# Kernel optimization log

Hardware: AMD Instinct MI355X
Metric: run time of the kernel (lower is better)

## Reference

```python
import jax, jax.numpy as jnp
import numpy as np

B, S, D, H, DH = 2, 1024, 1024, 16, 64
SCALE = 1.0 / np.sqrt(DH)


def setup_inputs() -> dict:
    key = jax.random.key(0)
    ks = jax.random.split(key, 9)
    return {
        "x": jax.random.normal(ks[0], (B, S, D), jnp.float32),
        "qkv_w": jax.random.normal(ks[1], (3 * H * DH, D), jnp.float32) * 0.02,
        "out_w": jax.random.normal(ks[2], (D, H * DH), jnp.float32) * 0.02,
        "bias_p": jax.random.uniform(ks[3], (H, 1, 1), jnp.float32) * 2.0,
        "bias_a": jax.random.uniform(ks[4], (H, 1, 1), jnp.float32),
        "mlp_w1": jax.random.normal(ks[5], (H, 2 * H), jnp.float32) * 0.1,
        "mlp_b1": jnp.zeros((H,), jnp.float32),
        "mlp_w2": jax.random.normal(ks[6], (H, H), jnp.float32) * 0.1,
        "mlp_b2": jnp.zeros((H,), jnp.float32),
    }


def reference(x, qkv_w, out_w, bias_p, bias_a, mlp_w1, mlp_b1, mlp_w2, mlp_b2):
    # qkv projection: torch Linear => x @ W.T
    qkv = (x @ qkv_w.T).reshape(B, S, 3, H, DH)
    q = qkv[:, :, 0].transpose(0, 2, 1, 3)  # [B,H,S,DH]
    k = qkv[:, :, 1].transpose(0, 2, 1, 3)
    v = qkv[:, :, 2].transpose(0, 2, 1, 3)

    scores = jnp.einsum('bhqd,bhkd->bhqk', q, k) * SCALE  # [B,H,S,S]

    # Kerple additive bias: -p * log1p(a * |i-j|), per head
    p = jnp.clip(bias_p, 0.01)
    a = jnp.clip(bias_a, 0.01)
    pos = jnp.arange(S, dtype=jnp.float32)
    dist = jnp.abs(pos[None, :] - pos[:, None])  # [S,S]
    kb = -p * jnp.log1p(a * dist)  # [H,S,S]

    # DAPE refinement MLP over per-(i,j) head features
    z = jnp.concatenate(
        [scores, jnp.broadcast_to(kb[None], (B, H, S, S))], axis=1
    ).transpose(0, 2, 3, 1)  # [B,S,S,2H]
    hdn = jax.nn.gelu(z @ mlp_w1.T + mlp_b1, approximate=False)  # [B,S,S,H]
    refine = (hdn @ mlp_w2.T + mlp_b2).transpose(0, 3, 1, 2)  # [B,H,S,S]

    scores = scores + kb[None] + refine
    attn = jax.nn.softmax(scores, axis=-1)  # dropout is identity in eval

    out = jnp.einsum('bhqk,bhkd->bhqd', attn, v)  # [B,H,S,DH]
    out = out.transpose(0, 2, 1, 3).reshape(B, S, H * DH)
    return out @ out_w.T
```

## Files before the change

### kernel.cpp

```cpp
#include <hip/hip_runtime.h>
#include <math.h>

#define Bsz 2
#define Ssz 1024
#define Dsz 1024
#define Hn 16
#define DHsz 64
#define QKV3 3072
#define SCALE 0.125f

typedef __bf16 bf16;
typedef bf16 bf16x8 __attribute__((ext_vector_type(8)));
typedef bf16 bf16x4 __attribute__((ext_vector_type(4)));
typedef float f32x4 __attribute__((ext_vector_type(4)));

#define MFMA(a, b, c) __builtin_amdgcn_mfma_f32_16x16x32_bf16(a, b, c, 0, 0, 0)
#define LDT 72

__global__ void cast_hi(const float* __restrict__ src, bf16* __restrict__ hi, int n) {
  int idx = (blockIdx.x * 256 + threadIdx.x) * 4;
  if (idx >= n) return;
  float4 v = *(const float4*)(src + idx);
  bf16x4 hv = {(bf16)v.x, (bf16)v.y, (bf16)v.z, (bf16)v.w};
  *(bf16x4*)(hi + idx) = hv;
}

__global__ void kb_table(const float* __restrict__ bias_p, const float* __restrict__ bias_a,
                         float* __restrict__ kbtt) {
  int idx = blockIdx.x * 256 + threadIdx.x;
  int d = idx >> 4, h = idx & 15;
  float p = fmaxf(bias_p[h], 0.01f), a = fmaxf(bias_a[h], 0.01f);
  kbtt[idx] = -p * log1pf(a * (float)d);
}

__global__ void tk_table(const float* __restrict__ kbtt, const float* __restrict__ w1,
                         const float* __restrict__ b1, float2* __restrict__ tk) {
  int idx = blockIdx.x * 256 + threadIdx.x;
  int o = idx >> 4, n = idx & 15;
  int d = o - 1024; if (d < 0) d = -d; if (d > 1023) d = 1023;
  float t1 = b1[n];
#pragma unroll
  for (int h = 0; h < 16; ++h) t1 += w1[n * 32 + 16 + h] * kbtt[d * 16 + h];
  tk[idx] = make_float2(t1, kbtt[d * 16 + n]);
}

__global__ void wfrag(const float* __restrict__ w1, const float* __restrict__ w2,
                      bf16* __restrict__ wf) {
  int lane = threadIdx.x;
  int l15 = lane & 15, q8 = (lane >> 4) << 3;
  bf16x8 w1d, w2a;
#pragma unroll
  for (int e = 0; e < 8; ++e) {
    int k = q8 + e;
    if (k < 16) {
      w1d[e] = (bf16)w1[l15 * 32 + k];
    } else {
      float w = w1[l15 * 32 + k - 16];
      w1d[e] = (bf16)(w - (float)(bf16)w);
    }
    w2a[e] = (bf16)w2[l15 * 16 + (k & 15)];
  }
  *(bf16x8*)(wf + lane * 8) = w1d;
  *(bf16x8*)(wf + 512 + lane * 8) = w2a;
}

__global__ __launch_bounds__(256, 3) void k1_qkv(const bf16* __restrict__ A,
                                                 const bf16* __restrict__ B,
                                                 bf16* __restrict__ C) {
  __shared__ __align__(16) bf16 sA[128 * LDT];
  __shared__ __align__(16) bf16 sB[96 * LDT];
  const int tid = threadIdx.x;
  const int lane = tid & 63, wv = tid >> 6;
  const int wr = wv >> 1, wc = wv & 1;
  const int l15 = lane & 15, q8 = (lane >> 4) << 3, q4 = (lane >> 4) << 2;
  const int m0 = blockIdx.y * 128, n0 = blockIdx.x * 96;
  const int r0 = tid >> 3, c8 = (tid & 7) << 3;

  f32x4 acc[4][3];
#pragma unroll
  for (int t = 0; t < 4; ++t)
#pragma unroll
    for (int u = 0; u < 3; ++u)
#pragma unroll
      for (int r = 0; r < 4; ++r) acc[t][u][r] = 0.f;

  bf16x8 rA[4], rB[3];
#define K1_LOAD(kt)                                                         \
  {                                                                         \
    _Pragma("unroll") for (int c = 0; c < 4; ++c)                           \
      rA[c] = *(const bf16x8*)(A + (size_t)(m0 + c * 32 + r0) * Dsz + (kt) + c8);  \
    _Pragma("unroll") for (int c = 0; c < 3; ++c)                           \
      rB[c] = *(const bf16x8*)(B + (size_t)(n0 + c * 32 + r0) * Dsz + (kt) + c8);  \
  }

  K1_LOAD(0)
  for (int kt = 0; kt < Dsz; kt += 64) {
    __syncthreads();
#pragma unroll
    for (int c = 0; c < 4; ++c) *(bf16x8*)&sA[(c * 32 + r0) * LDT + c8] = rA[c];
#pragma unroll
    for (int c = 0; c < 3; ++c) *(bf16x8*)&sB[(c * 32 + r0) * LDT + c8] = rB[c];
    __syncthreads();
    if (kt + 64 < Dsz) K1_LOAD(kt + 64)
#pragma unroll
    for (int ks = 0; ks < 64; ks += 32) {
      bf16x8 fa[4], fb[3];
#pragma unroll
      for (int t = 0; t < 4; ++t)
        fa[t] = *(const bf16x8*)&sA[(wr * 64 + t * 16 + l15) * LDT + ks + q8];
#pragma unroll
      for (int u = 0; u < 3; ++u)
        fb[u] = *(const bf16x8*)&sB[(wc * 48 + u * 16 + l15) * LDT + ks + q8];
#pragma unroll
      for (int t = 0; t < 4; ++t)
#pragma unroll
        for (int u = 0; u < 3; ++u) acc[t][u] = MFMA(fa[t], fb[u], acc[t][u]);
    }
  }
#pragma unroll
  for (int t = 0; t < 4; ++t)
#pragma unroll
    for (int u = 0; u < 3; ++u) {
      int col = n0 + wc * 48 + u * 16 + l15;
#pragma unroll
      for (int r = 0; r < 4; ++r) {
        int row = m0 + wr * 64 + t * 16 + q4 + r;
        C[(size_t)row * QKV3 + col] = (bf16)acc[t][u][r];
      }
    }
#undef K1_LOAD
}

__global__ void pack_vt(const bf16* __restrict__ qkv, bf16* __restrict__ vt) {
  __shared__ __align__(16) bf16 T[64 * LDT];
  const int tid = threadIdx.x;
  const int bh = blockIdx.y, b = bh >> 4, h = bh & 15;
  const int j0 = blockIdx.x * 64;
#pragma unroll
  for (int c = 0; c < 2; ++c) {
    int lin = c * 256 + tid;
    int jr = lin >> 3, d8 = (lin & 7) << 3;
    bf16x8 v = *(const bf16x8*)(qkv + (size_t)(b * Ssz + j0 + jr) * QKV3 + 2048 + h * DHsz + d8);
#pragma unroll
    for (int e = 0; e < 8; ++e) T[(d8 + e) * LDT + jr] = v[e];
  }
  __syncthreads();
#pragma unroll
  for (int c = 0; c < 2; ++c) {
    int lin = c * 256 + tid;
    int d = lin >> 3, j8 = (lin & 7) << 3;
    bf16x8 o = *(const bf16x8*)&T[d * LDT + j8];
    *(bf16x8*)(vt + ((size_t)(b * Hn + h) * DHsz + d) * Ssz + j0 + j8) = o;
  }
}

__global__ __launch_bounds__(256, 3) void k2_qk(const bf16* __restrict__ qkv,
                                                bf16* __restrict__ scores) {
  __shared__ __align__(16) bf16 sA[128 * LDT], sB[128 * LDT];
  const int tid = threadIdx.x;
  const int lane = tid & 63, wv = tid >> 6;
  const int wr = wv >> 1, wc = wv & 1;
  const int l15 = lane & 15, q8 = (lane >> 4) << 3, q4 = (lane >> 4) << 2;
  const int z = blockIdx.z, b = z >> 4, h = z & 15;
  const int i0 = blockIdx.y * 128, j0 = blockIdx.x * 128;
  const bf16* Ab = qkv + (size_t)b * Ssz * QKV3 + h * DHsz;
  const bf16* Bb = Ab + Ssz;
  const int r0 = tid >> 3, c8 = (tid & 7) << 3;
#pragma unroll
  for (int c = 0; c < 4; ++c) {
    int row = c * 32 + r0;
    *(bf16x8*)&sA[row * LDT + c8] = *(const bf16x8*)(Ab + (size_t)(i0 + row) * QKV3 + c8);
    *(bf16x8*)&sB[row * LDT + c8] = *(const bf16x8*)(Bb + (size_t)(j0 + row) * QKV3 + c8);
  }
  __syncthreads();
  f32x4 acc[4][4];
#pragma unroll
  for (int t = 0; t < 4; ++t)
#pragma unroll
    for (int u = 0; u < 4; ++u)
#pragma unroll
      for (int r = 0; r < 4; ++r) acc[t][u][r] = 0.f;
#pragma unroll
  for (int ks = 0; ks < 64; ks += 32) {
    bf16x8 fa[4], fb[4];
#pragma unroll
    for (int t = 0; t < 4; ++t) fa[t] = *(const bf16x8*)&sA[(wr * 64 + t * 16 + l15) * LDT + ks + q8];
#pragma unroll
    for (int u = 0; u < 4; ++u) fb[u] = *(const bf16x8*)&sB[(wc * 64 + u * 16 + l15) * LDT + ks + q8];
#pragma unroll
    for (int t = 0; t < 4; ++t)
#pragma unroll
      for (int u = 0; u < 4; ++u) acc[t][u] = MFMA(fa[t], fb[u], acc[t][u]);
  }
  bf16* dstp = scores + ((size_t)(b * Hn + h) << 20);
#pragma unroll
  for (int t = 0; t < 4; ++t)
#pragma unroll
    for (int u = 0; u < 4; ++u) {
      int col = j0 + wc * 64 + u * 16 + l15;
#pragma unroll
      for (int r = 0; r < 4; ++r) {
        int row = i0 + wr * 64 + t * 16 + q4 + r;
        dstp[((size_t)row << 10) + col] = (bf16)(acc[t][u][r] * SCALE);
      }
    }
}

__device__ __forceinline__ float gelu_fast(float x) {
  float z = fabsf(x) * 0.70710678118654752f;
  float t = __builtin_amdgcn_rcpf(fmaf(0.3275911f, z, 1.0f));
  float poly = t * fmaf(t, fmaf(t, fmaf(t, fmaf(t, 1.061405429f, -1.453152027f),
                                        1.421413741f), -0.284496736f), 0.254829592f);
  float erfa = 1.0f - poly * __expf(-z * z);
  float erfs = copysignf(erfa, x);
  return 0.5f * x * (1.0f + erfs);
}

#define SHS 264
#define LGS 264

__global__ __launch_bounds__(256, 5) void dape_softmax(bf16* scores,
                                                       const float2* __restrict__ tk,
                                                       const bf16* __restrict__ wf,
                                                       const float* __restrict__ b2,
                                                       float* __restrict__ sums) {
  const int c = blockIdx.x;
  const int i = blockIdx.y;
  const int b = blockIdx.z;
  const int tid = threadIdx.x;
  const int lane = tid & 63, wv = tid >> 6;
  const int l15 = lane & 15, q = lane >> 4;
  const int q8 = q << 3, q4 = q << 2;

  __shared__ bf16 sH[Hn][SHS];
  __shared__ float lgt[Hn][LGS];
  __shared__ __align__(16) bf16 hdnS[4][16][40];

  const bf16x8 w1d = *(const bf16x8*)(wf + lane * 8);
  const bf16x8 w2a = *(const bf16x8*)(wf + 512 + lane * 8);
  const float bias2 = b2[l15];

  if (lane < 32) {
    int row = lane >> 1, col = 16 + (lane & 1) * 8;
    *(bf16x8*)&hdnS[wv][row][col] = (bf16x8){};
  }

  const int jw = wv * 64;
  const bf16* srow = scores + ((size_t)(b * Hn) << 20) + ((size_t)i << 10) + c * 256;
#pragma unroll
  for (int t = 0; t < 2; ++t) {
    int h = t * 8 + (lane >> 3);
    int col = jw + (lane & 7) * 8;
    *(bf16x8*)&sH[h][col] = *(const bf16x8*)(srow + ((size_t)h << 20) + col);
  }

  const float2* tkp = tk + ((size_t)(c * 256 + jw + q4 - i + 1024) << 4) + l15;

  for (int jt = 0; jt < 4; ++jt) {
    const int j0c = jw + jt * 16;
    bf16x8 a1;
#pragma unroll
    for (int e = 0; e < 8; ++e) a1[e] = sH[(q8 + e) & 15][j0c + l15];
    float2 tkv[4];
#pragma unroll
    for (int r = 0; r < 4; ++r) tkv[r] = tkp[r * 16];
    f32x4 c1 = {tkv[0].x, tkv[1].x, tkv[2].x, tkv[3].x};
    c1 = MFMA(a1, w1d, c1);
#pragma unroll
    for (int r = 0; r < 4; ++r) hdnS[wv][q4 + r][l15] = (bf16)gelu_fast(c1[r]);
    bf16x8 a2 = *(const bf16x8*)&hdnS[wv][l15][q8];
    f32x4 c2 = {bias2, bias2, bias2, bias2};
    c2 = MFMA(a2, w2a, c2);
    bf16x4 sc4 = *(const bf16x4*)&sH[l15][j0c + q4];
    f32x4 lg;
#pragma unroll
    for (int r = 0; r < 4; ++r) lg[r] = (float)sc4[r] + tkv[r].y + c2[r];
    *(f32x4*)&lgt[l15][j0c + q4] = lg;
    tkp += 256;
  }
  __syncthreads();

#pragma unroll
  for (int hh = 0; hh < 4; ++hh) {
    const int h = wv * 4 + hh;
    f32x4 v0 = *(const f32x4*)&lgt[h][lane * 4];
    float s = 0.f;
#pragma unroll
    for (int e = 0; e < 4; ++e) { v0[e] = __expf(v0[e]); s += v0[e]; }
#pragma unroll
    for (int off = 32; off > 0; off >>= 1) s += __shfl_xor(s, off, 64);
    bf16* dst = scores + ((size_t)(b * Hn + h) << 20) + ((size_t)i << 10) + c * 256;
    bf16x4 p0 = {(bf16)v0[0], (bf16)v0[1], (bf16)v0[2], (bf16)v0[3]};
    *(bf16x4*)(dst + lane * 4) = p0;
    if (lane == 0) sums[((((b << 10) + i) << 4) + h) * 4 + c] = s;
  }
}

__global__ __launch_bounds__(256, 4) void k4_av(const bf16* __restrict__ attn,
                                                const bf16* __restrict__ vt,
                                                const float* __restrict__ sums,
                                                bf16* __restrict__ aout) {
  __shared__ __align__(16) bf16 sA[64 * LDT], sB[64 * LDT];
  const int tid = threadIdx.x;
  const int lane = tid & 63, wv = tid >> 6;
  const int wr = wv >> 1, wc = wv & 1;
  const int l15 = lane & 15, q8 = (lane >> 4) << 3, q4 = (lane >> 4) << 2;
  const int i0 = blockIdx.x * 64, h = blockIdx.y, b = blockIdx.z;
  const bf16* Ab = attn + ((size_t)(b * Hn + h) << 20) + ((size_t)i0 << 10);
  const bf16* Bb = vt + (size_t)(b * Hn + h) * DHsz * Ssz;
  const int r0 = tid >> 3, c8 = (tid & 7) << 3;
  f32x4 acc[2][2];
#pragma unroll
  for (int t = 0; t < 2; ++t)
#pragma unroll
    for (int u = 0; u < 2; ++u)
#pragma unroll
      for (int r = 0; r < 4; ++r) acc[t][u][r] = 0.f;
  bf16x8 rA[2], rB[2];
#define K4_LOAD(kt)                                               \
  {                                                               \
    _Pragma("unroll") for (int c = 0; c < 2; ++c) {               \
      int row = c * 32 + r0;                                      \
      rA[c] = *(const bf16x8*)(Ab + ((size_t)row << 10) + (kt) + c8); \
      rB[c] = *(const bf16x8*)(Bb + ((size_t)row << 10) + (kt) + c8); \
    }                                                             \
  }
  K4_LOAD(0)
  for (int kt = 0; kt < Ssz; kt += 64) {
    __syncthreads();
#pragma unroll
    for (int c = 0; c < 2; ++c) {
      int row = c * 32 + r0;
      *(bf16x8*)&sA[row * LDT + c8] = rA[c];
      *(bf16x8*)&sB[row * LDT + c8] = rB[c];
    }
    __syncthreads();
    if (kt + 64 < Ssz) K4_LOAD(kt + 64)
#pragma unroll
    for (int ks = 0; ks < 64; ks += 32) {
      bf16x8 fa[2], fb[2];
#pragma unroll
      for (int t = 0; t < 2; ++t) fa[t] = *(const bf16x8*)&sA[(wr * 32 + t * 16 + l15) * LDT + ks + q8];
#pragma unroll
      for (int u = 0; u < 2; ++u) fb[u] = *(const bf16x8*)&sB[(wc * 32 + u * 16 + l15) * LDT + ks + q8];
#pragma unroll
      for (int t = 0; t < 2; ++t)
#pragma unroll
        for (int u = 0; u < 2; ++u) acc[t][u] = MFMA(fa[t], fb[u], acc[t][u]);
    }
  }
#pragma unroll
  for (int t = 0; t < 2; ++t)
#pragma unroll
    for (int r = 0; r < 4; ++r) {
      int row = i0 + wr * 32 + t * 16 + q4 + r;
      f32x4 sv = *(const f32x4*)&sums[((((b << 10) + row) << 4) + h) * 4];
      float inv = 1.f / (sv[0] + sv[1] + sv[2] + sv[3]);
#pragma unroll
      for (int u = 0; u < 2; ++u) {
        int d = wc * 32 + u * 16 + l15;
        aout[(size_t)(b * Ssz + row) * Dsz + h * DHsz + d] = (bf16)(acc[t][u][r] * inv);
      }
    }
#undef K4_LOAD
}

__global__ __launch_bounds__(256, 4) void k5_out(const bf16* __restrict__ A,
                                                 const bf16* __restrict__ B,
                                                 float* __restrict__ C) {
  __shared__ __align__(16) bf16 sA[64 * LDT], sB[64 * LDT];
  const int tid = threadIdx.x;
  const int lane = tid & 63, wv = tid >> 6;
  const int wr = wv >> 1, wc = wv & 1;
  const int l15 = lane & 15, q8 = (lane >> 4) << 3, q4 = (lane >> 4) << 2;
  const int m0 = blockIdx.y * 64, n0 = blockIdx.x * 64;
  const int r0 = tid >> 3, c8 = (tid & 7) << 3;
  f32x4 acc[2][2];
#pragma unroll
  for (int t = 0; t < 2; ++t)
#pragma unroll
    for (int u = 0; u < 2; ++u)
#pragma unroll
      for (int r = 0; r < 4; ++r) acc[t][u][r] = 0.f;
  bf16x8 rA[2], rB[2];
#define K5_LOAD(kt)                                                       \
  {                                                                       \
    _Pragma("unroll") for (int c = 0; c < 2; ++c) {                       \
      int row = c * 32 + r0;                                              \
      rA[c] = *(const bf16x8*)(A + (size_t)(m0 + row) * Dsz + (kt) + c8);   \
      rB[c] = *(const bf16x8*)(B + (size_t)(n0 + row) * Dsz + (kt) + c8);   \
    }                                                                     \
  }
  K5_LOAD(0)
  for (int kt = 0; kt < Dsz; kt += 64) {
    __syncthreads();
#pragma unroll
    for (int c = 0; c < 2; ++c) {
      int row = c * 32 + r0;
      *(bf16x8*)&sA[row * LDT + c8] = rA[c];
      *(bf16x8*)&sB[row * LDT + c8] = rB[c];
    }
    __syncthreads();
    if (kt + 64 < Dsz) K5_LOAD(kt + 64)
#pragma unroll
    for (int ks = 0; ks < 64; ks += 32) {
      bf16x8 fa[2], fb[2];
#pragma unroll
      for (int t = 0; t < 2; ++t) fa[t] = *(const bf16x8*)&sA[(wr * 32 + t * 16 + l15) * LDT + ks + q8];
#pragma unroll
      for (int u = 0; u < 2; ++u) fb[u] = *(const bf16x8*)&sB[(wc * 32 + u * 16 + l15) * LDT + ks + q8];
#pragma unroll
      for (int t = 0; t < 2; ++t)
#pragma unroll
        for (int u = 0; u < 2; ++u) acc[t][u] = MFMA(fa[t], fb[u], acc[t][u]);
    }
  }
#pragma unroll
  for (int t = 0; t < 2; ++t)
#pragma unroll
    for (int u = 0; u < 2; ++u) {
      int col = n0 + wc * 32 + u * 16 + l15;
#pragma unroll
      for (int r = 0; r < 4; ++r) {
        int row = m0 + wr * 32 + t * 16 + q4 + r;
        C[(size_t)row * Dsz + col] = acc[t][u][r];
      }
    }
#undef K5_LOAD
}

extern "C" void kernel_launch(void* const* d_in, const int* in_sizes, int n_in,
                              void* d_out, int out_size, void* d_ws, size_t ws_size,
                              hipStream_t stream) {
  const float* x      = (const float*)d_in[0];
  const float* qkv_w  = (const float*)d_in[1];
  const float* out_w  = (const float*)d_in[2];
  const float* bias_p = (const float*)d_in[3];
  const float* bias_a = (const float*)d_in[4];
  const float* w1     = (const float*)d_in[5];
  const float* b1     = (const float*)d_in[6];
  const float* w2     = (const float*)d_in[7];
  const float* b2     = (const float*)d_in[8];
  float* out = (float*)d_out;

  char* ws = (char*)d_ws;
  const size_t MB = 1ull << 20;
  bf16* ow_h   = (bf16*)(ws + 0 * MB);
  bf16* qkv_bf = (bf16*)(ws + 2 * MB);
  bf16* v_t    = (bf16*)(ws + 14 * MB);
  bf16* aout   = (bf16*)(ws + 18 * MB);
  float* kbtt  = (float*)(ws + 22 * MB);
  float* sums  = (float*)(ws + 22 * MB + 65536);
  bf16* wf     = (bf16*)(ws + 22 * MB + 589824);
  float2* tk   = (float2*)(ws + 22 * MB + 655360);
  bf16* x_h    = (bf16*)(ws + 23 * MB);
  bf16* w_h    = (bf16*)(ws + 27 * MB);
  bf16* sc_bf  = (bf16*)(ws + 23 * MB);

  cast_hi<<<2048, 256, 0, stream>>>(x, x_h, Bsz * Ssz * Dsz);
  cast_hi<<<3072, 256, 0, stream>>>(qkv_w, w_h, QKV3 * Dsz);
  cast_hi<<<1024, 256, 0, stream>>>(out_w, ow_h, Dsz * Dsz);
  kb_table<<<64, 256, 0, stream>>>(bias_p, bias_a, kbtt);
  tk_table<<<128, 256, 0, stream>>>(kbtt, w1, b1, tk);
  wfrag<<<1, 64, 0, stream>>>(w1, w2, wf);

  k1_qkv<<<dim3(QKV3 / 96, (Bsz * Ssz) / 128), 256, 0, stream>>>(x_h, w_h, qkv_bf);
  pack_vt<<<dim3(Ssz / 64, Bsz * Hn), 256, 0, stream>>>(qkv_bf, v_t);

  k2_qk<<<dim3(Ssz / 128, Ssz / 128, Bsz * Hn), 256, 0, stream>>>(qkv_bf, sc_bf);
  dape_softmax<<<dim3(4, Ssz, Bsz), 256, 0, stream>>>(sc_bf, tk, wf, b2, sums);
  k4_av<<<dim3(Ssz / 64, Hn, Bsz), 256, 0, stream>>>(sc_bf, v_t, sums, aout);

  k5_out<<<dim3(Dsz / 64, (Bsz * Ssz) / 64), 256, 0, stream>>>(aout, ow_h, out);
}
```

Measured before the change: 202.9 us.

## Merge setup kernels and load GEMM fragments directly from global memory

Combines the three cast kernels into one launch and folds the kerple table, the tk table and the weight-fragment prep into a single kernel, which cuts six setup launches to two. The QK, AV and output-projection GEMMs now load MFMA fragments straight from global memory into registers and drop the LDS staging and __syncthreads. AV and the output projection double-buffer the next K tile in registers. This removes LDS traffic and barriers but gives up the coalesced cooperative loads, so global access patterns get more scattered and register pressure rises.

```diff
diff --git a/kernel.cpp b/kernel.cpp
--- a/kernel.cpp
+++ b/kernel.cpp
@@ -17,51 +17,60 @@
 #define MFMA(a, b, c) __builtin_amdgcn_mfma_f32_16x16x32_bf16(a, b, c, 0, 0, 0)
 #define LDT 72
 
-__global__ void cast_hi(const float* __restrict__ src, bf16* __restrict__ hi, int n) {
-  int idx = (blockIdx.x * 256 + threadIdx.x) * 4;
-  if (idx >= n) return;
+__global__ void cast3(const float* __restrict__ x, const float* __restrict__ qw,
+                      const float* __restrict__ ow, bf16* __restrict__ xh,
+                      bf16* __restrict__ wh, bf16* __restrict__ owh) {
+  int bid = blockIdx.x;
+  const float* src;
+  bf16* dst;
+  int base;
+  if (bid < 2048) { src = x;  dst = xh;  base = bid * 1024; }
+  else if (bid < 5120) { src = qw; dst = wh;  base = (bid - 2048) * 1024; }
+  else { src = ow; dst = owh; base = (bid - 5120) * 1024; }
+  int idx = base + threadIdx.x * 4;
   float4 v = *(const float4*)(src + idx);
   bf16x4 hv = {(bf16)v.x, (bf16)v.y, (bf16)v.z, (bf16)v.w};
-  *(bf16x4*)(hi + idx) = hv;
-}
-
-__global__ void kb_table(const float* __restrict__ bias_p, const float* __restrict__ bias_a,
-                         float* __restrict__ kbtt) {
-  int idx = blockIdx.x * 256 + threadIdx.x;
-  int d = idx >> 4, h = idx & 15;
-  float p = fmaxf(bias_p[h], 0.01f), a = fmaxf(bias_a[h], 0.01f);
-  kbtt[idx] = -p * log1pf(a * (float)d);
-}
-
-__global__ void tk_table(const float* __restrict__ kbtt, const float* __restrict__ w1,
-                         const float* __restrict__ b1, float2* __restrict__ tk) {
+  *(bf16x4*)(dst + idx) = hv;
+}
+
+__global__ void tkw(const float* __restrict__ bias_p, const float* __restrict__ bias_a,
+                    const float* __restrict__ w1, const float* __restrict__ b1,
+                    const float* __restrict__ w2, float2* __restrict__ tk,
+                    bf16* __restrict__ wf) {
+  if (blockIdx.x == 128) {
+    int lane = threadIdx.x;
+    if (lane < 64) {
+      int l15 = lane & 15, q8 = (lane >> 4) << 3;
+      bf16x8 w1d, w2a;
+#pragma unroll
+      for (int e = 0; e < 8; ++e) {
+        int k = q8 + e;
+        if (k < 16) {
+          w1d[e] = (bf16)w1[l15 * 32 + k];
+        } else {
+          float w = w1[l15 * 32 + k - 16];
+          w1d[e] = (bf16)(w - (float)(bf16)w);
+        }
+        w2a[e] = (bf16)w2[l15 * 16 + (k & 15)];
+      }
+      *(bf16x8*)(wf + lane * 8) = w1d;
+      *(bf16x8*)(wf + 512 + lane * 8) = w2a;
+    }
+    return;
+  }
   int idx = blockIdx.x * 256 + threadIdx.x;
   int o = idx >> 4, n = idx & 15;
   int d = o - 1024; if (d < 0) d = -d; if (d > 1023) d = 1023;
-  float t1 = b1[n];
-#pragma unroll
-  for (int h = 0; h < 16; ++h) t1 += w1[n * 32 + 16 + h] * kbtt[d * 16 + h];
-  tk[idx] = make_float2(t1, kbtt[d * 16 + n]);
-}
-
-__global__ void wfrag(const float* __restrict__ w1, const float* __restrict__ w2,
-                      bf16* __restrict__ wf) {
-  int lane = threadIdx.x;
-  int l15 = lane & 15, q8 = (lane >> 4) << 3;
-  bf16x8 w1d, w2a;
-#pragma unroll
-  for (int e = 0; e < 8; ++e) {
-    int k = q8 + e;
-    if (k < 16) {
-      w1d[e] = (bf16)w1[l15 * 32 + k];
-    } else {
-      float w = w1[l15 * 32 + k - 16];
-      w1d[e] = (bf16)(w - (float)(bf16)w);
-    }
-    w2a[e] = (bf16)w2[l15 * 16 + (k & 15)];
-  }
-  *(bf16x8*)(wf + lane * 8) = w1d;
-  *(bf16x8*)(wf + 512 + lane * 8) = w2a;
+  float dd = (float)d;
+  float t1 = b1[n], kbn = 0.f;
+#pragma unroll
+  for (int h = 0; h < 16; ++h) {
+    float p = fmaxf(bias_p[h], 0.01f), a = fmaxf(bias_a[h], 0.01f);
+    float kb = -p * log1pf(a * dd);
+    t1 += w1[n * 32 + 16 + h] * kb;
+    if (h == n) kbn = kb;
+  }
+  tk[idx] = make_float2(t1, kbn);
 }
 
 __global__ __launch_bounds__(256, 3) void k1_qkv(const bf16* __restrict__ A,
@@ -156,23 +165,23 @@
 
 __global__ __launch_bounds__(256, 3) void k2_qk(const bf16* __restrict__ qkv,
                                                 bf16* __restrict__ scores) {
-  __shared__ __align__(16) bf16 sA[128 * LDT], sB[128 * LDT];
   const int tid = threadIdx.x;
   const int lane = tid & 63, wv = tid >> 6;
   const int wr = wv >> 1, wc = wv & 1;
   const int l15 = lane & 15, q8 = (lane >> 4) << 3, q4 = (lane >> 4) << 2;
   const int z = blockIdx.z, b = z >> 4, h = z & 15;
   const int i0 = blockIdx.y * 128, j0 = blockIdx.x * 128;
-  const bf16* Ab = qkv + (size_t)b * Ssz * QKV3 + h * DHsz;
-  const bf16* Bb = Ab + Ssz;
-  const int r0 = tid >> 3, c8 = (tid & 7) << 3;
-#pragma unroll
-  for (int c = 0; c < 4; ++c) {
-    int row = c * 32 + r0;
-    *(bf16x8*)&sA[row * LDT + c8] = *(const bf16x8*)(Ab + (size_t)(i0 + row) * QKV3 + c8);
-    *(bf16x8*)&sB[row * LDT + c8] = *(const bf16x8*)(Bb + (size_t)(j0 + row) * QKV3 + c8);
-  }
-  __syncthreads();
+  const bf16* Ab = qkv + (size_t)(b * Ssz + i0 + wr * 64 + l15) * QKV3 + h * DHsz + q8;
+  const bf16* Bb = qkv + (size_t)(b * Ssz + j0 + wc * 64 + l15) * QKV3 + Ssz + h * DHsz + q8;
+
+  bf16x8 fa[2][4], fb[2][4];
+#pragma unroll
+  for (int s = 0; s < 2; ++s)
+#pragma unroll
+    for (int t = 0; t < 4; ++t) {
+      fa[s][t] = *(const bf16x8*)(Ab + (size_t)(t * 16) * QKV3 + s * 32);
+      fb[s][t] = *(const bf16x8*)(Bb + (size_t)(t * 16) * QKV3 + s * 32);
+    }
   f32x4 acc[4][4];
 #pragma unroll
   for (int t = 0; t < 4; ++t)
@@ -181,17 +190,12 @@
 #pragma unroll
       for (int r = 0; r < 4; ++r) acc[t][u][r] = 0.f;
 #pragma unroll
-  for (int ks = 0; ks < 64; ks += 32) {
-    bf16x8 fa[4], fb[4];
-#pragma unroll
-    for (int t = 0; t < 4; ++t) fa[t] = *(const bf16x8*)&sA[(wr * 64 + t * 16 + l15) * LDT + ks + q8];
-#pragma unroll
-    for (int u = 0; u < 4; ++u) fb[u] = *(const bf16x8*)&sB[(wc * 64 + u * 16 + l15) * LDT + ks + q8];
+  for (int s = 0; s < 2; ++s)
 #pragma unroll
     for (int t = 0; t < 4; ++t)
 #pragma unroll
-      for (int u = 0; u < 4; ++u) acc[t][u] = MFMA(fa[t], fb[u], acc[t][u]);
-  }
+      for (int u = 0; u < 4; ++u) acc[t][u] = MFMA(fa[s][t], fb[s][u], acc[t][u]);
+
   bf16* dstp = scores + ((size_t)(b * Hn + h) << 20);
 #pragma unroll
   for (int t = 0; t < 4; ++t)
@@ -300,15 +304,16 @@
                                                 const bf16* __restrict__ vt,
                                                 const float* __restrict__ sums,
                                                 bf16* __restrict__ aout) {
-  __shared__ __align__(16) bf16 sA[64 * LDT], sB[64 * LDT];
   const int tid = threadIdx.x;
   const int lane = tid & 63, wv = tid >> 6;
   const int wr = wv >> 1, wc = wv & 1;
   const int l15 = lane & 15, q8 = (lane >> 4) << 3, q4 = (lane >> 4) << 2;
   const int i0 = blockIdx.x * 64, h = blockIdx.y, b = blockIdx.z;
-  const bf16* Ab = attn + ((size_t)(b * Hn + h) << 20) + ((size_t)i0 << 10);
-  const bf16* Bb = vt + (size_t)(b * Hn + h) * DHsz * Ssz;
-  const int r0 = tid >> 3, c8 = (tid & 7) << 3;
+  const bf16* a0p = attn + ((size_t)(b * Hn + h) << 20) + ((size_t)(i0 + wr * 32 + l15) << 10) + q8;
+  const bf16* a1p = a0p + (16 << 10);
+  const bf16* b0p = vt + (size_t)(b * Hn + h) * DHsz * Ssz + ((size_t)(wc * 32 + l15) << 10) + q8;
+  const bf16* b1p = b0p + (16 << 10);
+
   f32x4 acc[2][2];
 #pragma unroll
   for (int t = 0; t < 2; ++t)
@@ -316,39 +321,34 @@
     for (int u = 0; u < 2; ++u)
 #pragma unroll
       for (int r = 0; r < 4; ++r) acc[t][u][r] = 0.f;
-  bf16x8 rA[2], rB[2];
-#define K4_LOAD(kt)                                               \
-  {                                                               \
-    _Pragma("unroll") for (int c = 0; c < 2; ++c) {               \
-      int row = c * 32 + r0;                                      \
-      rA[c] = *(const bf16x8*)(Ab + ((size_t)row << 10) + (kt) + c8); \
-      rB[c] = *(const bf16x8*)(Bb + ((size_t)row << 10) + (kt) + c8); \
-    }                                                             \
-  }
-  K4_LOAD(0)
+
+  bf16x8 ca[2][2], cb[2][2], na[2][2], nb[2][2];
+#define K4_LD(A_, B_, kt)                                 \
+  {                                                       \
+    _Pragma("unroll") for (int s = 0; s < 2; ++s) {       \
+      A_[s][0] = *(const bf16x8*)(a0p + (kt) + s * 32);   \
+      A_[s][1] = *(const bf16x8*)(a1p + (kt) + s * 32);   \
+      B_[s][0] = *(const bf16x8*)(b0p + (kt) + s * 32);   \
+      B_[s][1] = *(const bf16x8*)(b1p + (kt) + s * 32);   \
+    }                                                     \
+  }
+  K4_LD(ca, cb, 0)
   for (int kt = 0; kt < Ssz; kt += 64) {
-    __syncthreads();
-#pragma unroll
-    for (int c = 0; c < 2; ++c) {
-      int row = c * 32 + r0;
-      *(bf16x8*)&sA[row * LDT + c8] = rA[c];
-      *(bf16x8*)&sB[row * LDT + c8] = rB[c];
-    }
-    __syncthreads();
-    if (kt + 64 < Ssz) K4_LOAD(kt + 64)
-#pragma unroll
-    for (int ks = 0; ks < 64; ks += 32) {
-      bf16x8 fa[2], fb[2];
-#pragma unroll
-      for (int t = 0; t < 2; ++t) fa[t] = *(const bf16x8*)&sA[(wr * 32 + t * 16 + l15) * LDT + ks + q8];
-#pragma unroll
-      for (int u = 0; u < 2; ++u) fb[u] = *(const bf16x8*)&sB[(wc * 32 + u * 16 + l15) * LDT + ks + q8];
+    if (kt + 64 < Ssz) K4_LD(na, nb, kt + 64)
+#pragma unroll
+    for (int s = 0; s < 2; ++s)
 #pragma unroll
       for (int t = 0; t < 2; ++t)
 #pragma unroll
-        for (int u = 0; u < 2; ++u) acc[t][u] = MFMA(fa[t], fb[u], acc[t][u]);
-    }
-  }
+        for (int u = 0; u < 2; ++u) acc[t][u] = MFMA(ca[s][t], cb[s][u], acc[t][u]);
+    if (kt + 64 < Ssz) {
+#pragma unroll
+      for (int s = 0; s < 2; ++s)
+#pragma unroll
+        for (int t = 0; t < 2; ++t) { ca[s][t] = na[s][t]; cb[s][t] = nb[s][t]; }
+    }
+  }
+#undef K4_LD
 #pragma unroll
   for (int t = 0; t < 2; ++t)
 #pragma unroll
@@ -362,19 +362,21 @@
         aout[(size_t)(b * Ssz + row) * Dsz + h * DHsz + d] = (bf16)(acc[t][u][r] * inv);
       }
     }
-#undef K4_LOAD
 }
 
 __global__ __launch_bounds__(256, 4) void k5_out(const bf16* __restrict__ A,
                                                  const bf16* __restrict__ B,
                                                  float* __restrict__ C) {
-  __shared__ __align__(16) bf16 sA[64 * LDT], sB[64 * LDT];
   const int tid = threadIdx.x;
   const int lane = tid & 63, wv = tid >> 6;
   const int wr = wv >> 1, wc = wv & 1;
   const int l15 = lane & 15, q8 = (lane >> 4) << 3, q4 = (lane >> 4) << 2;
   const int m0 = blockIdx.y * 64, n0 = blockIdx.x * 64;
-  const int r0 = tid >> 3, c8 = (tid & 7) << 3;
+  const bf16* a0p = A + (size_t)(m0 + wr * 32 + l15) * Dsz + q8;
+  const bf16* a1p = a0p + 16 * Dsz;
+  const bf16* b0p = B + (size_t)(n0 + wc * 32 + l15) * Dsz + q8;
+  const bf16* b1p = b0p + 16 * Dsz;
+
   f32x4 acc[2][2];
 #pragma unroll
   for (int t = 0; t < 2; ++t)
@@ -382,39 +384,34 @@
     for (int u = 0; u < 2; ++u)
 #pragma unroll
       for (int r = 0; r < 4; ++r) acc[t][u][r] = 0.f;
-  bf16x8 rA[2], rB[2];
-#define K5_LOAD(kt)                                                       \
-  {                                                                       \
-    _Pragma("unroll") for (int c = 0; c < 2; ++c) {                       \
-      int row = c * 32 + r0;                                              \
-      rA[c] = *(const bf16x8*)(A + (size_t)(m0 + row) * Dsz + (kt) + c8);   \
-      rB[c] = *(const bf16x8*)(B + (size_t)(n0 + row) * Dsz + (kt) + c8);   \
-    }                                                                     \
-  }
-  K5_LOAD(0)
+
+  bf16x8 ca[2][2], cb[2][2], na[2][2], nb[2][2];
+#define K5_LD(A_, B_, kt)                                 \
+  {                                                       \
+    _Pragma("unroll") for (int s = 0; s < 2; ++s) {       \
+      A_[s][0] = *(const bf16x8*)(a0p + (kt) + s * 32);   \
+      A_[s][1] = *(const bf16x8*)(a1p + (kt) + s * 32);   \
+      B_[s][0] = *(const bf16x8*)(b0p + (kt) + s * 32);   \
+      B_[s][1] = *(const bf16x8*)(b1p + (kt) + s * 32);   \
+    }                                                     \
+  }
+  K5_LD(ca, cb, 0)
   for (int kt = 0; kt < Dsz; kt += 64) {
-    __syncthreads();
-#pragma unroll
-    for (int c = 0; c < 2; ++c) {
-      int row = c * 32 + r0;
-      *(bf16x8*)&sA[row * LDT + c8] = rA[c];
-      *(bf16x8*)&sB[row * LDT + c8] = rB[c];
-    }
-    __syncthreads();
-    if (kt + 64 < Dsz) K5_LOAD(kt + 64)
-#pragma unroll
-    for (int ks = 0; ks < 64; ks += 32) {
-      bf16x8 fa[2], fb[2];
-#pragma unroll
-      for (int t = 0; t < 2; ++t) fa[t] = *(const bf16x8*)&sA[(wr * 32 + t * 16 + l15) * LDT + ks + q8];
-#pragma unroll
-      for (int u = 0; u < 2; ++u) fb[u] = *(const bf16x8*)&sB[(wc * 32 + u * 16 + l15) * LDT + ks + q8];
+    if (kt + 64 < Dsz) K5_LD(na, nb, kt + 64)
+#pragma unroll
+    for (int s = 0; s < 2; ++s)
 #pragma unroll
       for (int t = 0; t < 2; ++t)
 #pragma unroll
-        for (int u = 0; u < 2; ++u) acc[t][u] = MFMA(fa[t], fb[u], acc[t][u]);
-    }
-  }
+        for (int u = 0; u < 2; ++u) acc[t][u] = MFMA(ca[s][t], cb[s][u], acc[t][u]);
+    if (kt + 64 < Dsz) {
+#pragma unroll
+      for (int s = 0; s < 2; ++s)
+#pragma unroll
+        for (int t = 0; t < 2; ++t) { ca[s][t] = na[s][t]; cb[s][t] = nb[s][t]; }
+    }
+  }
+#undef K5_LD
 #pragma unroll
   for (int t = 0; t < 2; ++t)
 #pragma unroll
@@ -426,7 +423,6 @@
         C[(size_t)row * Dsz + col] = acc[t][u][r];
       }
     }
-#undef K5_LOAD
 }
 
 extern "C" void kernel_launch(void* const* d_in, const int* in_sizes, int n_in,
@@ -449,20 +445,15 @@
   bf16* qkv_bf = (bf16*)(ws + 2 * MB);
   bf16* v_t    = (bf16*)(ws + 14 * MB);
   bf16* aout   = (bf16*)(ws + 18 * MB);
-  float* kbtt  = (float*)(ws + 22 * MB);
-  float* sums  = (float*)(ws + 22 * MB + 65536);
-  bf16* wf     = (bf16*)(ws + 22 * MB + 589824);
-  float2* tk   = (float2*)(ws + 22 * MB + 655360);
+  float* sums  = (float*)(ws + 22 * MB);
+  bf16* wf     = (bf16*)(ws + 22 * MB + 524288);
+  float2* tk   = (float2*)(ws + 22 * MB + 589824);
   bf16* x_h    = (bf16*)(ws + 23 * MB);
   bf16* w_h    = (bf16*)(ws + 27 * MB);
   bf16* sc_bf  = (bf16*)(ws + 23 * MB);
 
-  cast_hi<<<2048, 256, 0, stream>>>(x, x_h, Bsz * Ssz * Dsz);
-  cast_hi<<<3072, 256, 0, stream>>>(qkv_w, w_h, QKV3 * Dsz);
-  cast_hi<<<1024, 256, 0, stream>>>(out_w, ow_h, Dsz * Dsz);
-  kb_table<<<64, 256, 0, stream>>>(bias_p, bias_a, kbtt);
-  tk_table<<<128, 256, 0, stream>>>(kbtt, w1, b1, tk);
-  wfrag<<<1, 64, 0, stream>>>(w1, w2, wf);
+  cast3<<<6144, 256, 0, stream>>>(x, qkv_w, out_w, x_h, w_h, ow_h);
+  tkw<<<129, 256, 0, stream>>>(bias_p, bias_a, w1, b1, w2, tk, wf);
 
   k1_qkv<<<dim3(QKV3 / 96, (Bsz * Ssz) / 128), 256, 0, stream>>>(x_h, w_h, qkv_bf);
   pack_vt<<<dim3(Ssz / 64, Bsz * Hn), 256, 0, stream>>>(qkv_bf, v_t);
```

Measured after the change: 240.6 us. +18.6%, slower.
